# Kernel tuning notes

Hardware: AMD Instinct MI355X
Metric: run time of the kernel (lower is better)

Reference implementation:

```python
import jax, jax.numpy as jnp
import numpy as np

TEMPERATURE = 1.0  # init kwarg
B, D = 8192, 128


def setup_inputs() -> dict:
    key = jax.random.key(0)
    k1, k2 = jax.random.split(key)
    sk = jax.random.normal(k1, (B, D), dtype=jnp.float32)
    im = jax.random.normal(k2, (B, D), dtype=jnp.float32)
    return {"sk": sk, "im": im}


def reference(sk, im):
    # The torch module builds a [2B,2B] Euclidean distance matrix over the
    # interleaved [sk_0, im_0, sk_1, im_1, ...] rows, then via the eye-mask /
    # repeat_interleave / [:,1::2] / good_indices / [::2] gather chain selects,
    # for each anchor i, logits row = [-d(sk_i, im_i)/T] ++ [-d(sk_i, im_j)/T, j != i]
    # with label 0, followed by mean cross-entropy.  Since cross-entropy only
    # depends on {row values} and which entry is positive, this is exactly:
    #   loss = mean_i( logsumexp_j(-d(sk_i, im_j)/T) - (-d(sk_i, im_i)/T) )
    # so we only need the [B,B] sk-vs-im distance block (dist_type == 0).
    sq = (
        jnp.sum(sk * sk, axis=1)[:, None]
        + jnp.sum(im * im, axis=1)[None, :]
        - 2.0 * (sk @ im.T)
    )  # [B, B] squared distances
    d = jnp.sqrt(jnp.maximum(sq, 0.0))
    logits = -d / TEMPERATURE  # [B, B]
    lse = jax.nn.logsumexp(logits, axis=1)  # [B]
    loss = jnp.mean(lse - jnp.diagonal(logits))
    return loss
```

## Files before the change

kernel.cpp:

```cpp
#include <hip/hip_runtime.h>
#include <math.h>

#define NB 8192
#define ND 128
#define NJB 64

#define C2F 2.0813689810056077f
#define NC2 (-4.1627379620112154f)

typedef __bf16 bf16x8 __attribute__((ext_vector_type(8)));
typedef float f32x4 __attribute__((ext_vector_type(4)));

typedef __attribute__((address_space(3))) void lds_void_t;
typedef __attribute__((address_space(1))) const void gconst_void_t;

__device__ __forceinline__ unsigned f2bf(float f) {
    union { float f; unsigned u; } v; v.f = f;
    unsigned r = v.u + 0x7FFFu + ((v.u >> 16) & 1u);
    return r >> 16;
}

__global__ void __launch_bounds__(256) prep_kernel(
    const float* __restrict__ sk, const float* __restrict__ im,
    unsigned short* __restrict__ skb, unsigned short* __restrict__ imb,
    float* __restrict__ skn, float* __restrict__ imn,
    float* __restrict__ diag, float* __restrict__ gacc,
    unsigned* __restrict__ ticket) {
    if (blockIdx.x == 0 && threadIdx.x == 0) { *gacc = 0.f; *ticket = 0u; }
    const int wave = threadIdx.x >> 6, lane = threadIdx.x & 63;
    const int half = lane >> 5, l32 = lane & 31;
    const int row = blockIdx.x * 8 + wave * 2 + half;
    const size_t off = (size_t)row * ND + l32 * 4;
    const float4 a = *reinterpret_cast<const float4*>(sk + off);
    const float4 b = *reinterpret_cast<const float4*>(im + off);
    ushort4 pa, pb;
    pa.x = (unsigned short)f2bf(a.x); pa.y = (unsigned short)f2bf(a.y);
    pa.z = (unsigned short)f2bf(a.z); pa.w = (unsigned short)f2bf(a.w);
    pb.x = (unsigned short)f2bf(b.x); pb.y = (unsigned short)f2bf(b.y);
    pb.z = (unsigned short)f2bf(b.z); pb.w = (unsigned short)f2bf(b.w);
    *reinterpret_cast<ushort4*>(skb + off) = pa;
    *reinterpret_cast<ushort4*>(imb + off) = pb;
    float sa = a.x * a.x + a.y * a.y + a.z * a.z + a.w * a.w;
    float sb = b.x * b.x + b.y * b.y + b.z * b.z + b.w * b.w;
    float dx = a.x - b.x, dy = a.y - b.y, dz = a.z - b.z, dw = a.w - b.w;
    float sd = dx * dx + dy * dy + dz * dz + dw * dw;
#pragma unroll
    for (int st = 1; st < 32; st <<= 1) {
        sa += __shfl_xor(sa, st);
        sb += __shfl_xor(sb, st);
        sd += __shfl_xor(sd, st);
    }
    if (l32 == 0) {
        skn[row] = sa * C2F;
        imn[row] = sb * C2F;
        diag[row] = sqrtf(sd);
    }
}

__global__ void __launch_bounds__(512, 4) tile_kernel(
    const unsigned short* __restrict__ skb, const unsigned short* __restrict__ imb,
    const float* __restrict__ skn, const float* __restrict__ imn,
    float* __restrict__ partial) {
    __shared__ unsigned short tiles[256 * 128];
    __shared__ float lds_part[2][128];

    const int t = threadIdx.x;
    const int w = t >> 6, lane = t & 63;
    const int hi = lane >> 4, lo = lane & 15;
    const int tI = blockIdx.x * 128;
    const int tJ = blockIdx.y * 128;

    {
        const unsigned short* gsrc = (w < 4) ? imb : skb;
        const int grow0 = ((w < 4) ? tJ : tI) + (w & 3) * 32;
        unsigned short* ldst = tiles + (size_t)w * 32 * ND;
#pragma unroll
        for (int q = 0; q < 8; ++q) {
            const int rl = q * 4 + hi;
            const int cs = lo ^ (rl & 15);
            const unsigned short* gp = gsrc + (size_t)(grow0 + rl) * ND + cs * 8;
            __builtin_amdgcn_global_load_lds((gconst_void_t*)gp,
                                             (lds_void_t*)(ldst + q * 4 * ND),
                                             16, 0, 0);
        }
    }

    const int wr = w >> 2, wc = w & 3;
    const int ibase = tI + wc * 32;
    const int jbase = tJ + wr * 64;

    float skv2[2];
#pragma unroll
    for (int n = 0; n < 2; ++n) skv2[n] = skn[ibase + n * 16 + lo];
    float imnv2[4][4];
#pragma unroll
    for (int m = 0; m < 4; ++m) {
        float4 v = *reinterpret_cast<const float4*>(imn + jbase + m * 16 + hi * 4);
        imnv2[m][0] = v.x; imnv2[m][1] = v.y; imnv2[m][2] = v.z; imnv2[m][3] = v.w;
    }

    __syncthreads();

    f32x4 acc[4][2];
#pragma unroll
    for (int m = 0; m < 4; ++m)
#pragma unroll
        for (int n = 0; n < 2; ++n)
            acc[m][n] = (f32x4){0.f, 0.f, 0.f, 0.f};

    const char* Tb = (const char*)tiles;
#pragma unroll
    for (int kk = 0; kk < 4; ++kk) {
        const int cb = ((kk * 4 + hi) ^ lo) << 4;
        bf16x8 af[4], bfr[2];
#pragma unroll
        for (int m = 0; m < 4; ++m)
            af[m] = *reinterpret_cast<const bf16x8*>(Tb + (wr * 64 + m * 16 + lo) * 256 + cb);
#pragma unroll
        for (int n = 0; n < 2; ++n)
            bfr[n] = *reinterpret_cast<const bf16x8*>(Tb + (128 + wc * 32 + n * 16 + lo) * 256 + cb);
#pragma unroll
        for (int m = 0; m < 4; ++m)
#pragma unroll
            for (int n = 0; n < 2; ++n)
                acc[m][n] = __builtin_amdgcn_mfma_f32_16x16x32_bf16(af[m], bfr[n], acc[m][n], 0, 0, 0);
    }

#pragma unroll
    for (int n = 0; n < 2; ++n) {
        float s = 0.f;
#pragma unroll
        for (int m = 0; m < 4; ++m) {
#pragma unroll
            for (int r = 0; r < 4; ++r) {
                float sq2 = fmaf(NC2, acc[m][n][r], skv2[n]) + imnv2[m][r];
                sq2 = fmaxf(sq2, 0.f);
                float d2;
                asm("v_sqrt_f32 %0, %1" : "=v"(d2) : "v"(sq2));
                float e;
                asm("v_exp_f32 %0, -%1" : "=v"(e) : "v"(d2));
                s += e;
            }
        }
        s += __shfl_xor(s, 16);
        s += __shfl_xor(s, 32);
        if (lane < 16) lds_part[wr][wc * 32 + n * 16 + lane] = s;
    }
    __syncthreads();
    if (t < 128)
        partial[(size_t)(tI + t) * NJB + blockIdx.y] =
            lds_part[0][t] + lds_part[1][t];
}

__global__ void finalize_kernel(const float* __restrict__ partial,
                                const float* __restrict__ diag,
                                float* __restrict__ gacc, unsigned* __restrict__ ticket,
                                float* __restrict__ out) {
    const int i = blockIdx.x * 256 + threadIdx.x;
    const float4* p4 = reinterpret_cast<const float4*>(partial + (size_t)i * NJB);
    float rs = 0.f;
#pragma unroll
    for (int q = 0; q < NJB / 4; ++q) {
        float4 v = p4[q];
        rs += (v.x + v.y) + (v.z + v.w);
    }
    float v = __logf(rs) + diag[i];
    __shared__ float red[256];
    red[threadIdx.x] = v;
    __syncthreads();
    for (int st = 128; st > 0; st >>= 1) {
        if (threadIdx.x < st) red[threadIdx.x] += red[threadIdx.x + st];
        __syncthreads();
    }
    if (threadIdx.x == 0) {
        atomicAdd(gacc, red[0]);
        __threadfence();
        unsigned old = atomicAdd(ticket, 1u);
        if (old == (NB / 256) - 1) {
            float tot = atomicAdd(gacc, 0.f);
            out[0] = tot / (float)NB;
        }
    }
}

extern "C" void kernel_launch(void* const* d_in, const int* in_sizes, int n_in,
                              void* d_out, int out_size, void* d_ws, size_t ws_size,
                              hipStream_t stream) {
    const float* sk = (const float*)d_in[0];
    const float* im = (const float*)d_in[1];
    float* out = (float*)d_out;
    float* ws = (float*)d_ws;

    unsigned short* skb = (unsigned short*)ws;
    unsigned short* imb = skb + (size_t)NB * ND;
    float* fbase   = ws + (size_t)NB * ND;
    float* skn     = fbase;
    float* imn     = fbase + NB;
    float* diag    = fbase + 2 * NB;
    float* partial = fbase + 3 * NB;
    float* gacc    = partial + (size_t)NB * NJB;
    unsigned* ticket = (unsigned*)(gacc + 1);

    prep_kernel<<<NB / 8, 256, 0, stream>>>(
        sk, im, skb, imb, skn, imn, diag, gacc, ticket);
    dim3 grid(NB / 128, NB / 128);
    tile_kernel<<<grid, 512, 0, stream>>>(skb, imb, skn, imn, partial);
    finalize_kernel<<<NB / 256, 256, 0, stream>>>(partial, diag, gacc, ticket, out);
}
```

Baseline: 98.04 us.

## Keep sk fragments in registers and stream double-buffered im tiles through LDS

Each wave now owns 64 sk rows whose bf16 fragments are loaded once into registers. The block streams four 64-row im tiles through a double-buffered LDS stage, accumulating exp-sums across the j steps in registers. This replaces the 128x128 one-shot tile per block, so the grid shrinks from 4096 to 512 blocks and there are fewer partials, stored column-major for coalesced finalize reads. In exchange it uses more registers (launch bounds drop to 2 blocks per CU), leaves fewer blocks to spread across CUs, and adds intra-block syncs per step.

```diff
diff --git a/kernel.cpp b/kernel.cpp
--- a/kernel.cpp
+++ b/kernel.cpp
@@ -3,7 +3,9 @@
 
 #define NB 8192
 #define ND 128
-#define NJB 64
+#define GSTEP 64
+#define NSTEP 4
+#define NJB 32
 
 #define C2F 2.0813689810056077f
 #define NC2 (-4.1627379620112154f)
@@ -57,99 +59,114 @@
     }
 }
 
-__global__ void __launch_bounds__(512, 4) tile_kernel(
+__global__ void __launch_bounds__(512, 2) tile_kernel(
     const unsigned short* __restrict__ skb, const unsigned short* __restrict__ imb,
     const float* __restrict__ skn, const float* __restrict__ imn,
     float* __restrict__ partial) {
-    __shared__ unsigned short tiles[256 * 128];
-    __shared__ float lds_part[2][128];
+    __shared__ unsigned short Ast[2][GSTEP * ND];
 
     const int t = threadIdx.x;
     const int w = t >> 6, lane = t & 63;
     const int hi = lane >> 4, lo = lane & 15;
-    const int tI = blockIdx.x * 128;
-    const int tJ = blockIdx.y * 128;
-
-    {
-        const unsigned short* gsrc = (w < 4) ? imb : skb;
-        const int grow0 = ((w < 4) ? tJ : tI) + (w & 3) * 32;
-        unsigned short* ldst = tiles + (size_t)w * 32 * ND;
-#pragma unroll
-        for (int q = 0; q < 8; ++q) {
-            const int rl = q * 4 + hi;
-            const int cs = lo ^ (rl & 15);
-            const unsigned short* gp = gsrc + (size_t)(grow0 + rl) * ND + cs * 8;
-            __builtin_amdgcn_global_load_lds((gconst_void_t*)gp,
-                                             (lds_void_t*)(ldst + q * 4 * ND),
-                                             16, 0, 0);
-        }
-    }
-
-    const int wr = w >> 2, wc = w & 3;
-    const int ibase = tI + wc * 32;
-    const int jbase = tJ + wr * 64;
-
-    float skv2[2];
-#pragma unroll
-    for (int n = 0; n < 2; ++n) skv2[n] = skn[ibase + n * 16 + lo];
-    float imnv2[4][4];
-#pragma unroll
-    for (int m = 0; m < 4; ++m) {
-        float4 v = *reinterpret_cast<const float4*>(imn + jbase + m * 16 + hi * 4);
-        imnv2[m][0] = v.x; imnv2[m][1] = v.y; imnv2[m][2] = v.z; imnv2[m][3] = v.w;
-    }
-
+    const int iw = blockIdx.x * 512 + w * 64;
+    const int jg0 = blockIdx.y * (GSTEP * NSTEP);
+
+    bf16x8 bfr[4][4];
+#pragma unroll
+    for (int n = 0; n < 4; ++n) {
+        const unsigned short* bp = skb + (size_t)(iw + n * 16 + lo) * ND + hi * 8;
+#pragma unroll
+        for (int kk = 0; kk < 4; ++kk)
+            bfr[n][kk] = *reinterpret_cast<const bf16x8*>(bp + kk * 32);
+    }
+    float skv[4];
+#pragma unroll
+    for (int n = 0; n < 4; ++n) skv[n] = skn[iw + n * 16 + lo];
+
+#define STAGE_A(buf, jrow0)                                                     \
+    {                                                                           \
+        _Pragma("unroll")                                                       \
+        for (int q = 0; q < 2; ++q) {                                           \
+            const int rl = w * 8 + q * 4 + hi;                                  \
+            const int cs = lo ^ (rl & 15);                                      \
+            const unsigned short* gp = imb + (size_t)((jrow0) + rl) * ND + cs * 8; \
+            __builtin_amdgcn_global_load_lds((gconst_void_t*)gp,                \
+                (lds_void_t*)(&Ast[(buf)][(w * 8 + q * 4) * ND]), 16, 0, 0);    \
+        }                                                                       \
+    }
+
+    STAGE_A(0, jg0)
     __syncthreads();
 
-    f32x4 acc[4][2];
-#pragma unroll
-    for (int m = 0; m < 4; ++m)
-#pragma unroll
-        for (int n = 0; n < 2; ++n)
-            acc[m][n] = (f32x4){0.f, 0.f, 0.f, 0.f};
-
-    const char* Tb = (const char*)tiles;
-#pragma unroll
-    for (int kk = 0; kk < 4; ++kk) {
-        const int cb = ((kk * 4 + hi) ^ lo) << 4;
-        bf16x8 af[4], bfr[2];
+    float sacc[4] = {0.f, 0.f, 0.f, 0.f};
+
+#pragma unroll
+    for (int s = 0; s < NSTEP; ++s) {
+        const int jb = jg0 + s * GSTEP;
+        if (s + 1 < NSTEP) STAGE_A((s + 1) & 1, jb + GSTEP)
+
+        float imnv[4][4];
+#pragma unroll
+        for (int m = 0; m < 4; ++m) {
+            float4 v = *reinterpret_cast<const float4*>(imn + jb + m * 16 + hi * 4);
+            imnv[m][0] = v.x; imnv[m][1] = v.y; imnv[m][2] = v.z; imnv[m][3] = v.w;
+        }
+
+        f32x4 acc[4][4];
 #pragma unroll
         for (int m = 0; m < 4; ++m)
-            af[m] = *reinterpret_cast<const bf16x8*>(Tb + (wr * 64 + m * 16 + lo) * 256 + cb);
-#pragma unroll
-        for (int n = 0; n < 2; ++n)
-            bfr[n] = *reinterpret_cast<const bf16x8*>(Tb + (128 + wc * 32 + n * 16 + lo) * 256 + cb);
-#pragma unroll
-        for (int m = 0; m < 4; ++m)
-#pragma unroll
-            for (int n = 0; n < 2; ++n)
-                acc[m][n] = __builtin_amdgcn_mfma_f32_16x16x32_bf16(af[m], bfr[n], acc[m][n], 0, 0, 0);
-    }
-
-#pragma unroll
-    for (int n = 0; n < 2; ++n) {
-        float s = 0.f;
-#pragma unroll
-        for (int m = 0; m < 4; ++m) {
-#pragma unroll
-            for (int r = 0; r < 4; ++r) {
-                float sq2 = fmaf(NC2, acc[m][n][r], skv2[n]) + imnv2[m][r];
-                sq2 = fmaxf(sq2, 0.f);
-                float d2;
-                asm("v_sqrt_f32 %0, %1" : "=v"(d2) : "v"(sq2));
-                float e;
-                asm("v_exp_f32 %0, -%1" : "=v"(e) : "v"(d2));
-                s += e;
+#pragma unroll
+            for (int n = 0; n < 4; ++n)
+                acc[m][n] = (f32x4){0.f, 0.f, 0.f, 0.f};
+
+        const char* Ab = (const char*)Ast[s & 1];
+#pragma unroll
+        for (int kk = 0; kk < 4; ++kk) {
+            const int cb = ((kk * 4 + hi) ^ lo) << 4;
+            bf16x8 af[4];
+#pragma unroll
+            for (int m = 0; m < 4; ++m)
+                af[m] = *reinterpret_cast<const bf16x8*>(Ab + (m * 16 + lo) * 256 + cb);
+#pragma unroll
+            for (int m = 0; m < 4; ++m)
+#pragma unroll
+                for (int n = 0; n < 4; ++n)
+                    acc[m][n] = __builtin_amdgcn_mfma_f32_16x16x32_bf16(
+                        af[m], bfr[n][kk], acc[m][n], 0, 0, 0);
+        }
+
+#pragma unroll
+        for (int n = 0; n < 4; ++n) {
+            float ssum = 0.f;
+#pragma unroll
+            for (int m = 0; m < 4; ++m) {
+#pragma unroll
+                for (int r = 0; r < 4; ++r) {
+                    float sq2 = fmaf(NC2, acc[m][n][r], skv[n]) + imnv[m][r];
+                    sq2 = fmaxf(sq2, 0.f);
+                    float d2;
+                    asm("v_sqrt_f32 %0, %1" : "=v"(d2) : "v"(sq2));
+                    float e;
+                    asm("v_exp_f32 %0, -%1" : "=v"(e) : "v"(d2));
+                    ssum += e;
+                }
             }
-        }
-        s += __shfl_xor(s, 16);
-        s += __shfl_xor(s, 32);
-        if (lane < 16) lds_part[wr][wc * 32 + n * 16 + lane] = s;
-    }
-    __syncthreads();
-    if (t < 128)
-        partial[(size_t)(tI + t) * NJB + blockIdx.y] =
-            lds_part[0][t] + lds_part[1][t];
+            sacc[n] += ssum;
+        }
+        if (s + 1 < NSTEP) __syncthreads();
+    }
+
+#pragma unroll
+    for (int n = 0; n < 4; ++n) {
+        sacc[n] += __shfl_xor(sacc[n], 16);
+        sacc[n] += __shfl_xor(sacc[n], 32);
+    }
+    if (lane < 16) {
+#pragma unroll
+        for (int n = 0; n < 4; ++n)
+            partial[(size_t)blockIdx.y * NB + iw + n * 16 + lo] = sacc[n];
+    }
+#undef STAGE_A
 }
 
 __global__ void finalize_kernel(const float* __restrict__ partial,
@@ -157,13 +174,9 @@
                                 float* __restrict__ gacc, unsigned* __restrict__ ticket,
                                 float* __restrict__ out) {
     const int i = blockIdx.x * 256 + threadIdx.x;
-    const float4* p4 = reinterpret_cast<const float4*>(partial + (size_t)i * NJB);
     float rs = 0.f;
 #pragma unroll
-    for (int q = 0; q < NJB / 4; ++q) {
-        float4 v = p4[q];
-        rs += (v.x + v.y) + (v.z + v.w);
-    }
+    for (int c = 0; c < NJB; ++c) rs += partial[(size_t)c * NB + i];
     float v = __logf(rs) + diag[i];
     __shared__ float red[256];
     red[threadIdx.x] = v;
@@ -198,12 +211,12 @@
     float* imn     = fbase + NB;
     float* diag    = fbase + 2 * NB;
     float* partial = fbase + 3 * NB;
-    float* gacc    = partial + (size_t)NB * NJB;
+    float* gacc    = partial + (size_t)NJB * NB;
     unsigned* ticket = (unsigned*)(gacc + 1);
 
     prep_kernel<<<NB / 8, 256, 0, stream>>>(
         sk, im, skb, imb, skn, imn, diag, gacc, ticket);
-    dim3 grid(NB / 128, NB / 128);
+    dim3 grid(NB / 512, NB / (GSTEP * NSTEP));
     tile_kernel<<<grid, 512, 0, stream>>>(skb, imb, skn, imn, partial);
     finalize_kernel<<<NB / 256, 256, 0, stream>>>(partial, diag, gacc, ticket, out);
 }
```

After: 98.45 us. Within noise of the previous version (+0.4%).
